# Kernel optimization log

Measured on AMD Instinct MI355X. Metric: run time of the kernel, lower is better.

## Reference

```python
import jax, jax.numpy as jnp
import numpy as np

B, K, H_IMG, W_IMG = 8, 1, 512, 512
N_ITR = 10      # fixed iteration count (torch max_itr loop, unrolled via scan)
TOL = 1e-3      # convergence tolerance used for per-element gating


def setup_inputs() -> dict:
    key = jax.random.key(0)
    k1, k2 = jax.random.split(key)
    img = jax.random.normal(k1, (B, K, H_IMG, W_IMG), dtype=jnp.float32)
    temp = jax.random.normal(k2, (B, K, H_IMG, W_IMG), dtype=jnp.float32)
    return {"img": img, "temp": temp}


def _grad_batch(F):
    # central difference with replicate padding (== conv with [-0.5,0,0.5])
    px = jnp.pad(F, ((0, 0), (0, 0), (0, 0), (1, 1)), mode='edge')
    dx = 0.5 * (px[..., 2:] - px[..., :-2])
    py = jnp.pad(F, ((0, 0), (0, 0), (1, 1), (0, 0)), mode='edge')
    dy = 0.5 * (py[..., 2:, :] - py[..., :-2, :])
    return dx, dy


def _bilinear_sample(img, xp, yp):
    # img [B,k,h,w]; xp,yp pixel coords [B,h,w]; zeros padding, align_corners=True
    _, k, h, w = img.shape
    x0 = jnp.floor(xp)
    y0 = jnp.floor(yp)
    wx1 = xp - x0
    wy1 = yp - y0

    def tap(xi, yi, wgt):
        valid = (xi >= 0) & (xi <= w - 1) & (yi >= 0) & (yi <= h - 1)
        xc = jnp.clip(xi, 0, w - 1).astype(jnp.int32)
        yc = jnp.clip(yi, 0, h - 1).astype(jnp.int32)
        v = jax.vmap(lambda im, yy, xx: im[:, yy, xx])(img, yc, xc)  # [B,k,h,w]
        return v * (wgt * valid.astype(img.dtype))[:, None]

    return (tap(x0, y0, (1 - wx1) * (1 - wy1)) + tap(x0 + 1, y0, wx1 * (1 - wy1))
            + tap(x0, y0 + 1, (1 - wx1) * wy1) + tap(x0 + 1, y0 + 1, wx1 * wy1))


def _deeplk(img, temp):
    Bb, k, h, w = temp.shape
    gx, gy = _grad_batch(temp)
    # centered pixel coordinates (meshgrid with x - x.max()/2)
    xs = jnp.arange(w, dtype=jnp.float32) - (w - 1) / 2.0
    ys = jnp.arange(h, dtype=jnp.float32) - (h - 1) / 2.0
    X, Y = jnp.meshgrid(xs, ys)  # each [h,w]
    Xf = jnp.tile(X.reshape(-1), k)  # [k*h*w]
    Yf = jnp.tile(Y.reshape(-1), k)
    gxf = gx.reshape(Bb, -1)
    gyf = gy.reshape(Bb, -1)
    # Jacobian dI/dp: [B, k*h*w, 8]
    dIdp = jnp.stack([
        Xf * gxf, Yf * gxf, gxf,
        Xf * gyf, Yf * gyf, gyf,
        -Xf * Xf * gxf - Xf * Yf * gyf,
        -Xf * Yf * gxf - Yf * Yf * gyf], axis=-1)
    Hm = jnp.einsum('bni,bnj->bij', dIdp, dIdp)        # [B,8,8]
    invH = jnp.linalg.inv(Hm)
    invH_dIdp = jnp.einsum('bij,bnj->bin', invH, dIdp)  # [B,8,N]

    xy1 = jnp.stack([X.reshape(-1), Y.reshape(-1),
                     jnp.ones(h * w, jnp.float32)], axis=0)  # [3, h*w]
    I3 = jnp.eye(3, dtype=jnp.float32)

    def param_to_H(p):
        return I3 + jnp.concatenate([p, jnp.zeros((Bb, 1), p.dtype)], 1).reshape(Bb, 3, 3)

    def step(carry, _):
        p, dp = carry  # p,dp: [B,8]
        Hh = param_to_H(p)
        xyw = jnp.einsum('bij,jn->bin', Hh, xy1)
        Xw = (xyw[:, 0] / xyw[:, 2]).reshape(Bb, h, w) + (w - 1) / 2.0
        Yw = (xyw[:, 1] / xyw[:, 2]).reshape(Bb, h, w) + (h - 1) / 2.0
        Fi_warp = _bilinear_sample(img, Xw, Yw)
        xn = Xw / ((w - 1) / 2.0) - 1.0
        yn = Yw / ((h - 1) / 2.0) - 1.0
        mask = ((xn > -1 + 2.0 / w) & (xn < 1 - 2.0 / w) &
                (yn > -1 + 2.0 / h) & (yn < 1 - 2.0 / h)).astype(img.dtype)
        r = (Fi_warp - temp * mask[:, None]).reshape(Bb, -1)  # [B,N]
        dp_new = jnp.einsum('bin,bn->bi', invH_dIdp, r)       # [B,8]
        dp_new = dp_new.at[:, 6:8].set(0.0)                   # no projective update
        gate = (jnp.linalg.norm(dp, axis=1, keepdims=True) > TOL).astype(p.dtype)
        dp_next = gate * dp_new
        return (p - dp_next, dp_next), None

    p0 = jnp.zeros((Bb, 8), jnp.float32)
    dp0 = jnp.ones((Bb, 8), jnp.float32)
    (p, _), _ = jax.lax.scan(step, (p0, dp0), None, length=N_ITR)
    return p.reshape(Bb, 8, 1), param_to_H(p)


def reference(img, temp):
    return _deeplk(img, temp)
```

## Files before the change

### kernel.cpp

```cpp
#include <hip/hip_runtime.h>
#include <math.h>

#define W     512
#define HH    512
#define NB    8
#define NBLK  512
#define TPB   512
#define NW    (TPB / 64)
#define BPB   64
#define ROWS  8
#define NPX   (ROWS * W)
#define PXT   (NPX / TPB)
#define NITR  10
#define POISON64 0xAAAAAAAAAAAAAAAAull
#define ALL64  0xFFFFFFFFFFFFFFFFull
#define MLO 0.998046875f
#define MHI 510.001953125f

__device__ __forceinline__ float wave_reduce8(float x) {
    x += __shfl_down(x, 32, 64);
    x += __shfl_down(x, 16, 64);
    x += __shfl_down(x, 8, 64);
    return x;
}
__device__ __forceinline__ double red8_d(double x) {
    x += __shfl_down(x, 32, 64);
    x += __shfl_down(x, 16, 64);
    x += __shfl_down(x, 8, 64);
    return x;
}
__device__ __forceinline__ double load_d(const double* p) {
    unsigned long long u = __hip_atomic_load((const unsigned long long*)p,
                       __ATOMIC_RELAXED, __HIP_MEMORY_SCOPE_AGENT);
    return __builtin_bit_cast(double, u);
}
__device__ __forceinline__ void store_d(double* p, double v) {
    __hip_atomic_store((unsigned long long*)p, __builtin_bit_cast(unsigned long long, v),
                       __ATOMIC_RELAXED, __HIP_MEMORY_SCOPE_AGENT);
}
__device__ __forceinline__ bool not_poison(double v) {
    return __builtin_bit_cast(unsigned long long, v) != POISON64;
}

__device__ __forceinline__ float hrec(int t, float X1, float X2, float X3, float X4,
    float a0, float a1, float a2, float b0, float b1, float b2, float b3,
    float c0, float c1, float c2, float c3, float c4)
{
    switch (t) {
    case 0:  return X2 * a0;             case 1:  return X1 * a1;
    case 2:  return X1 * a0;             case 3:  return X2 * b0;
    case 4:  return X1 * b1;             case 5:  return X1 * b0;
    case 6:  return -(X3 * a0 + X2 * b1);
    case 7:  return -(X2 * a1 + X1 * b2);
    case 8:  return a2;                  case 9:  return a1;
    case 10: return X1 * b1;             case 11: return b2;
    case 12: return b1;
    case 13: return -(X2 * a1 + X1 * b2);
    case 14: return -(X1 * a2 + b3);
    case 15: return a0;                  case 16: return X1 * b0;
    case 17: return b1;                  case 18: return b0;
    case 19: return -(X2 * a0 + X1 * b1);
    case 20: return -(X1 * a1 + b2);
    case 21: return X2 * c0;             case 22: return X1 * c1;
    case 23: return X1 * c0;
    case 24: return -(X3 * b0 + X2 * c1);
    case 25: return -(X2 * b1 + X1 * c2);
    case 26: return c2;                  case 27: return c1;
    case 28: return -(X2 * b1 + X1 * c2);
    case 29: return -(X1 * b2 + c3);
    case 30: return c0;
    case 31: return -(X2 * b0 + X1 * c1);
    case 32: return -(X1 * b1 + c2);
    case 33: return X4 * a0 + 2.f * X3 * b1 + X2 * c2;
    case 34: return X3 * a1 + 2.f * X2 * b2 + X1 * c3;
    default: return X2 * a2 + 2.f * X1 * b3 + c4;
    }
}

extern "C" __global__ __launch_bounds__(TPB, 4)
void deeplk_kernel(const float* __restrict__ img, const float* __restrict__ temp,
                   float* __restrict__ out, void* __restrict__ wsv)
{
    double* Hpart = (double*)wsv;
    double* vpart = Hpart + NB * 36 * BPB;

    const int tid   = threadIdx.x;
    const int lane  = tid & 63;
    const int wv    = tid >> 6;
    const int b     = blockIdx.x & 7;
    const int chunk = blockIdx.x >> 3;
    const int row0  = chunk * ROWS;
    const float* tb = temp + b * (HH * W);
    const float* ib = img  + b * (HH * W);

    float rgx[PXT], rgy[PXT], rtv[PXT];

    __shared__ float  s_h8[64 * 36];
    __shared__ float  s_h2[8 * 36];
    __shared__ double s_Hu[36];
    __shared__ double s_invH[64];
    __shared__ double s_p[8], s_dp[8], s_v[8];
    __shared__ double s_vred[8 * 8];

    const float X1 = (float)tid - 255.5f;

    float a0 = 0.f, a1 = 0.f, a2 = 0.f;
    float b0 = 0.f, b1 = 0.f, b2 = 0.f, b3 = 0.f;
    float c0 = 0.f, c1 = 0.f, c2 = 0.f, c3 = 0.f, c4 = 0.f;
    float A = 0.f, Bv = 0.f, Cv = 0.f, Dv = 0.f, Ev = 0.f;
    {
        const int cc = tid;
        const int cl = (cc > 0) ? cc - 1 : 0;
        const int cr = (cc < W - 1) ? cc + 1 : W - 1;
        const bool xm = (cc >= 1) && (cc <= 510);
        float Yv = (float)row0 - 255.5f;
#pragma unroll
        for (int u = 0; u < PXT; ++u) {
            const int rr = row0 + u;
            const int ru = (rr > 0) ? rr - 1 : 0;
            const int rd = (rr < HH - 1) ? rr + 1 : HH - 1;
            const float gx = 0.5f * (tb[rr * W + cr] - tb[rr * W + cl]);
            const float gy = 0.5f * (tb[rd * W + cc] - tb[ru * W + cc]);
            const float tc = tb[rr * W + cc];
            rgx[u] = gx; rgy[u] = gy; rtv[u] = tc;
            const float q1 = gx * gx, q2 = gx * gy, q3 = gy * gy;
            const float y2 = Yv * Yv, y3 = y2 * Yv, y4 = y2 * y2;
            a0 += q1; a1 += Yv * q1; a2 += y2 * q1;
            b0 += q2; b1 += Yv * q2; b2 += y2 * q2; b3 += y3 * q2;
            c0 += q3; c1 += Yv * q3; c2 += y2 * q3; c3 += y3 * q3; c4 += y4 * q3;
            const float m  = (xm && rr >= 1 && rr <= 510) ? 1.f : 0.f;
            const float rv = ib[rr * W + cc] - tc * m;
            const float t1 = gx * rv, t2 = gy * rv;
            A  += t1;        Bv += t2;
            Cv += Yv * t1;   Dv += Yv * t2;
            Ev += y2 * t2;
            Yv += 1.f;
        }
    }
    {
        const float X2 = X1 * X1, X3 = X2 * X1, X4 = X2 * X2;
#pragma unroll
        for (int t = 0; t < 36; ++t) {
            float x = wave_reduce8(hrec(t, X1, X2, X3, X4,
                                        a0, a1, a2, b0, b1, b2, b3,
                                        c0, c1, c2, c3, c4));
            if (lane < 8) s_h8[(wv * 8 + lane) * 36 + t] = x;
        }
        __syncthreads();
        if (tid < 288) {
            const int g = tid / 36, t = tid % 36;
            float s = 0.f;
#pragma unroll
            for (int w2 = 0; w2 < 8; ++w2) s += s_h8[(w2 * 8 + g) * 36 + t];
            s_h2[g * 36 + t] = s;
        }
        __syncthreads();
        if (tid < 36) {
            double s = 0.0;
#pragma unroll
            for (int g = 0; g < 8; ++g) s += (double)s_h2[g * 36 + tid];
            store_d(&Hpart[(b * 36 + tid) * BPB + chunk], s);
        }
        __syncthreads();
        float va[8];
        va[0] = X1 * A;  va[1] = Cv;  va[2] = A;
        va[3] = X1 * Bv; va[4] = Dv;  va[5] = Bv;
        va[6] = -(X1 * X1 * A + X1 * Dv);
        va[7] = -(X1 * Cv + Ev);
#pragma unroll
        for (int c = 0; c < 8; ++c) {
            float x = wave_reduce8(va[c]);
            if (lane < 8) s_h8[(wv * 8 + lane) * 8 + c] = x;
        }
        __syncthreads();
        if (tid < 64) {
            const int g = tid >> 3, c = tid & 7;
            float s = 0.f;
#pragma unroll
            for (int w2 = 0; w2 < 8; ++w2) s += s_h8[(w2 * 8 + g) * 8 + c];
            s_h2[g * 8 + c] = s;
        }
        __syncthreads();
        if (tid < 8) {
            double s = 0.0;
#pragma unroll
            for (int g = 0; g < 8; ++g) s += (double)s_h2[g * 8 + tid];
            store_d(&vpart[b * BPB * 8 + chunk * 8 + tid], s);
        }
    }
    for (int c = wv; c < 36; c += NW) {
        const double* hp = &Hpart[(b * 36 + c) * BPB + lane];
        double x;
        for (;;) {
            x = load_d(hp);
            if (__ballot(not_poison(x)) == ALL64) break;
            __builtin_amdgcn_s_sleep(1);
        }
        x += __shfl_down(x, 32, 64);
        x += __shfl_down(x, 16, 64);
        x += __shfl_down(x, 8, 64);
        x += __shfl_down(x, 4, 64);
        x += __shfl_down(x, 2, 64);
        x += __shfl_down(x, 1, 64);
        if (lane == 0) s_Hu[c] = x;
    }
    {
        const double* slot = &vpart[b * BPB * 8 + tid];
        double x;
        for (;;) {
            x = load_d(slot);
            if (__ballot(not_poison(x)) == ALL64) break;
            __builtin_amdgcn_s_sleep(1);
        }
        x += __shfl_down(x, 32, 64);
        x += __shfl_down(x, 16, 64);
        x += __shfl_down(x, 8, 64);
        if (lane < 8) s_vred[wv * 8 + lane] = x;
    }
    __syncthreads();
    if (tid < 8) {
        double s = 0.0;
#pragma unroll
        for (int w2 = 0; w2 < NW; ++w2) s += s_vred[w2 * 8 + tid];
        s_v[tid] = s;
    }
    __syncthreads();

    if (tid < 64) {
        const int r  = tid >> 3, cj = tid & 7;
        const int i2 = (r < cj) ? r : cj;
        const int j2 = (r < cj) ? cj : r;
        double a = s_Hu[i2 * 8 - (i2 * (i2 - 1)) / 2 + (j2 - i2)];
        double e = (r == cj) ? 1.0 : 0.0;
#pragma unroll
        for (int k = 0; k < 8; ++k) {
            int pr = k;
            double pv = fabs(__shfl(a, k * 8 + k, 64));
            for (int rr2 = k + 1; rr2 < 8; ++rr2) {
                double c = fabs(__shfl(a, rr2 * 8 + k, 64));
                if (c > pv) { pv = c; pr = rr2; }
            }
            double a_k = __shfl(a, k * 8 + cj, 64),  e_k = __shfl(e, k * 8 + cj, 64);
            double a_p = __shfl(a, pr * 8 + cj, 64), e_p = __shfl(e, pr * 8 + cj, 64);
            if (r == k)       { a = a_p; e = e_p; }
            else if (r == pr) { a = a_k; e = e_k; }
            double piv = __shfl(a, k * 8 + k, 64);
            double d = 1.0 / piv;
            if (r == k) { a *= d; e *= d; }
            double f  = __shfl(a, r * 8 + k, 64);
            double ak = __shfl(a, k * 8 + cj, 64);
            double ek = __shfl(e, k * 8 + cj, 64);
            if (r != k) { a -= f * ak; e -= f * ek; }
        }
        s_invH[tid] = e;
    }
    __syncthreads();
    if (tid < 8) {
        double dpn = 0.0;
#pragma unroll
        for (int l = 0; l < 8; ++l) dpn += s_invH[tid * 8 + l] * s_v[l];
        if (tid >= 6) dpn = 0.0;
        s_p[tid]  = -dpn;
        s_dp[tid] = dpn;
    }
    __syncthreads();

    for (int it = 1; it < NITR; ++it) {
        double n2 = 0.0;
#pragma unroll
        for (int l = 0; l < 8; ++l) { double d = s_dp[l]; n2 += d * d; }
        if (n2 > 1e-6) {
            const float a00 = 1.f + (float)s_p[0];
            const float a01 = (float)s_p[1];
            const float a02 = (float)s_p[2] + 255.5f;
            const float a10 = (float)s_p[3];
            const float a11 = 1.f + (float)s_p[4];
            const float a12 = (float)s_p[5] + 255.5f;
            float Yv = (float)row0 - 255.5f;
            float Xw = a00 * X1 + a01 * Yv + a02;
            float Yw = a10 * X1 + a11 * Yv + a12;
            float Ai = 0.f, Bi = 0.f, Ci = 0.f, Di = 0.f, Ei = 0.f;

#pragma unroll
            for (int u = 0; u < PXT; ++u) {
                const float xf = floorf(Xw), yf = floorf(Yw);
                const int ix = (int)xf, iy = (int)yf;
                const float wx = Xw - xf, wy = Yw - yf;
                const bool vx0 = (ix >= 0) & (ix < W);
                const bool vx1 = (ix >= -1) & (ix < W - 1);
                const bool vy0 = (iy >= 0) & (iy < HH);
                const bool vy1 = (iy >= -1) & (iy < HH - 1);
                const float* ro0 = ib + iy * W;
                const float* ro1 = ro0 + W;
                const float t00 = (vx0 && vy0) ? ro0[ix]     : 0.f;
                const float t10 = (vx1 && vy0) ? ro0[ix + 1] : 0.f;
                const float t01 = (vx0 && vy1) ? ro1[ix]     : 0.f;
                const float t11 = (vx1 && vy1) ? ro1[ix + 1] : 0.f;
                const float omx = 1.f - wx, omy = 1.f - wy;
                const float Fi = (t00 * omx + t10 * wx) * omy
                               + (t01 * omx + t11 * wx) * wy;
                const float m = (Xw > MLO && Xw < MHI && Yw > MLO && Yw < MHI) ? 1.f : 0.f;
                const float rv = Fi - rtv[u] * m;
                const float t1 = rgx[u] * rv, t2 = rgy[u] * rv;
                Ai += t1;        Bi += t2;
                Ci += Yv * t1;   Di += Yv * t2;
                Ei += (Yv * Yv) * t2;
                Xw += a01; Yw += a11; Yv += 1.f;
            }
            float va[8];
            {
                const float X2 = X1 * X1;
                va[0] = X1 * Ai; va[1] = Ci;  va[2] = Ai;
                va[3] = X1 * Bi; va[4] = Di;  va[5] = Bi;
                va[6] = -(X2 * Ai + X1 * Di);
                va[7] = -(X1 * Ci + Ei);
            }
#pragma unroll
            for (int c = 0; c < 8; ++c) {
                float x = wave_reduce8(va[c]);
                if (lane < 8) s_h8[(wv * 8 + lane) * 8 + c] = x;
            }
            __syncthreads();
            double* vp = vpart + ((it * NB) + b) * BPB * 8;
            if (wv == 0) {
                const int g2 = lane >> 3, c2 = lane & 7;
                double s = 0.0;
#pragma unroll
                for (int j = 0; j < 8; ++j) s += (double)s_h8[(j * 8 + g2) * 8 + c2];
                s = red8_d(s);
                if (lane < 8) store_d(&vp[chunk * 8 + lane], s);
            }
            {
                const double* slot = &vp[tid];
                double x;
                for (;;) {
                    x = load_d(slot);
                    if (__ballot(not_poison(x)) == ALL64) break;
                    __builtin_amdgcn_s_sleep(1);
                }
                x += __shfl_down(x, 32, 64);
                x += __shfl_down(x, 16, 64);
                x += __shfl_down(x, 8, 64);
                if (lane < 8) s_vred[wv * 8 + lane] = x;
            }
            __syncthreads();
            if (tid < 8) {
                double s = 0.0;
#pragma unroll
                for (int w2 = 0; w2 < NW; ++w2) s += s_vred[w2 * 8 + tid];
                s_v[tid] = s;
                double dpn = 0.0;
#pragma unroll
                for (int l = 0; l < 8; ++l) dpn += s_invH[tid * 8 + l] * s_v[l];
                if (tid >= 6) dpn = 0.0;
                s_p[tid] -= dpn;
                s_dp[tid] = dpn;
            }
            __syncthreads();
        }
    }

    if (chunk == 0) {
        if (tid < 8) out[b * 8 + tid] = (float)s_p[tid];
        if (tid == 0) {
            float* Ho = out + 64 + b * 9;
            Ho[0] = 1.f + (float)s_p[0]; Ho[1] = (float)s_p[1];       Ho[2] = (float)s_p[2];
            Ho[3] = (float)s_p[3];       Ho[4] = 1.f + (float)s_p[4]; Ho[5] = (float)s_p[5];
            Ho[6] = (float)s_p[6];       Ho[7] = (float)s_p[7];       Ho[8] = 1.f;
        }
    }
}

extern "C" void kernel_launch(void* const* d_in, const int* in_sizes, int n_in,
                              void* d_out, int out_size, void* d_ws, size_t ws_size,
                              hipStream_t stream) {
    const float* img  = (const float*)d_in[0];
    const float* temp = (const float*)d_in[1];
    float* out = (float*)d_out;
    void*  ws  = d_ws;
    void* args[] = { &img, &temp, &out, &ws };
    hipError_t e = hipLaunchCooperativeKernel((const void*)deeplk_kernel, dim3(NBLK),
                                              dim3(TPB), args, 0, stream);
    if (e != hipSuccess) {
        deeplk_kernel<<<dim3(NBLK), dim3(TPB), 0, stream>>>(img, temp, out, ws);
    }
}
```

Before: 152.0 us.

## Use 256 blocks of 1024 threads, each covering 16 rows

Halves the number of cooperating blocks by doubling the threads per block. Each block now covers 16 rows, split into two 8-row halves by thread index. The per-iteration cross-block spin-wait reduction then polls 32 partial slots per batch instead of 64, and the in-block reductions over 16 waves are adjusted to match. The aim is to cut global synchronisation and polling cost across the 10 iterations, at the price of fewer, larger blocks with higher register pressure. Launch bounds stay at (TPB, 4), so occupancy and register allocation may change.

```diff
diff --git a/kernel.cpp b/kernel.cpp
--- a/kernel.cpp
+++ b/kernel.cpp
@@ -4,11 +4,11 @@
 #define W     512
 #define HH    512
 #define NB    8
-#define NBLK  512
-#define TPB   512
+#define NBLK  256
+#define TPB   1024
 #define NW    (TPB / 64)
-#define BPB   64
-#define ROWS  8
+#define BPB   32
+#define ROWS  16
 #define NPX   (ROWS * W)
 #define PXT   (NPX / TPB)
 #define NITR  10
@@ -89,34 +89,35 @@
     const int wv    = tid >> 6;
     const int b     = blockIdx.x & 7;
     const int chunk = blockIdx.x >> 3;
-    const int row0  = chunk * ROWS;
+    const int cc    = tid & 511;
+    const int half  = tid >> 9;
+    const int rbase = chunk * ROWS + half * 8;
     const float* tb = temp + b * (HH * W);
     const float* ib = img  + b * (HH * W);
 
     float rgx[PXT], rgy[PXT], rtv[PXT];
 
-    __shared__ float  s_h8[64 * 36];
+    __shared__ float  s_h8[128 * 36];
     __shared__ float  s_h2[8 * 36];
     __shared__ double s_Hu[36];
     __shared__ double s_invH[64];
     __shared__ double s_p[8], s_dp[8], s_v[8];
     __shared__ double s_vred[8 * 8];
 
-    const float X1 = (float)tid - 255.5f;
+    const float X1 = (float)cc - 255.5f;
 
     float a0 = 0.f, a1 = 0.f, a2 = 0.f;
     float b0 = 0.f, b1 = 0.f, b2 = 0.f, b3 = 0.f;
     float c0 = 0.f, c1 = 0.f, c2 = 0.f, c3 = 0.f, c4 = 0.f;
     float A = 0.f, Bv = 0.f, Cv = 0.f, Dv = 0.f, Ev = 0.f;
     {
-        const int cc = tid;
         const int cl = (cc > 0) ? cc - 1 : 0;
         const int cr = (cc < W - 1) ? cc + 1 : W - 1;
         const bool xm = (cc >= 1) && (cc <= 510);
-        float Yv = (float)row0 - 255.5f;
+        float Yv = (float)rbase - 255.5f;
 #pragma unroll
         for (int u = 0; u < PXT; ++u) {
-            const int rr = row0 + u;
+            const int rr = rbase + u;
             const int ru = (rr > 0) ? rr - 1 : 0;
             const int rd = (rr < HH - 1) ? rr + 1 : HH - 1;
             const float gx = 0.5f * (tb[rr * W + cr] - tb[rr * W + cl]);
@@ -151,7 +152,7 @@
             const int g = tid / 36, t = tid % 36;
             float s = 0.f;
 #pragma unroll
-            for (int w2 = 0; w2 < 8; ++w2) s += s_h8[(w2 * 8 + g) * 36 + t];
+            for (int w2 = 0; w2 < 16; ++w2) s += s_h8[(w2 * 8 + g) * 36 + t];
             s_h2[g * 36 + t] = s;
         }
         __syncthreads();
@@ -177,7 +178,7 @@
             const int g = tid >> 3, c = tid & 7;
             float s = 0.f;
 #pragma unroll
-            for (int w2 = 0; w2 < 8; ++w2) s += s_h8[(w2 * 8 + g) * 8 + c];
+            for (int w2 = 0; w2 < 16; ++w2) s += s_h8[(w2 * 8 + g) * 8 + c];
             s_h2[g * 8 + c] = s;
         }
         __syncthreads();
@@ -189,14 +190,14 @@
         }
     }
     for (int c = wv; c < 36; c += NW) {
-        const double* hp = &Hpart[(b * 36 + c) * BPB + lane];
+        const double* hp = &Hpart[(b * 36 + c) * BPB + (lane & 31)];
         double x;
         for (;;) {
             x = load_d(hp);
             if (__ballot(not_poison(x)) == ALL64) break;
             __builtin_amdgcn_s_sleep(1);
         }
-        x += __shfl_down(x, 32, 64);
+        if (lane >= 32) x = 0.0;
         x += __shfl_down(x, 16, 64);
         x += __shfl_down(x, 8, 64);
         x += __shfl_down(x, 4, 64);
@@ -204,7 +205,7 @@
         x += __shfl_down(x, 1, 64);
         if (lane == 0) s_Hu[c] = x;
     }
-    {
+    if (tid < 256) {
         const double* slot = &vpart[b * BPB * 8 + tid];
         double x;
         for (;;) {
@@ -212,16 +213,14 @@
             if (__ballot(not_poison(x)) == ALL64) break;
             __builtin_amdgcn_s_sleep(1);
         }
-        x += __shfl_down(x, 32, 64);
-        x += __shfl_down(x, 16, 64);
-        x += __shfl_down(x, 8, 64);
+        x = red8_d(x);
         if (lane < 8) s_vred[wv * 8 + lane] = x;
     }
     __syncthreads();
     if (tid < 8) {
         double s = 0.0;
 #pragma unroll
-        for (int w2 = 0; w2 < NW; ++w2) s += s_vred[w2 * 8 + tid];
+        for (int w2 = 0; w2 < 4; ++w2) s += s_vred[w2 * 8 + tid];
         s_v[tid] = s;
     }
     __syncthreads();
@@ -276,7 +275,7 @@
             const float a10 = (float)s_p[3];
             const float a11 = 1.f + (float)s_p[4];
             const float a12 = (float)s_p[5] + 255.5f;
-            float Yv = (float)row0 - 255.5f;
+            float Yv = (float)rbase - 255.5f;
             float Xw = a00 * X1 + a01 * Yv + a02;
             float Yw = a10 * X1 + a11 * Yv + a12;
             float Ai = 0.f, Bi = 0.f, Ci = 0.f, Di = 0.f, Ei = 0.f;
@@ -326,11 +325,11 @@
                 const int g2 = lane >> 3, c2 = lane & 7;
                 double s = 0.0;
 #pragma unroll
-                for (int j = 0; j < 8; ++j) s += (double)s_h8[(j * 8 + g2) * 8 + c2];
+                for (int j = 0; j < 16; ++j) s += (double)s_h8[(j * 8 + g2) * 8 + c2];
                 s = red8_d(s);
                 if (lane < 8) store_d(&vp[chunk * 8 + lane], s);
             }
-            {
+            if (tid < 256) {
                 const double* slot = &vp[tid];
                 double x;
                 for (;;) {
@@ -338,16 +337,14 @@
                     if (__ballot(not_poison(x)) == ALL64) break;
                     __builtin_amdgcn_s_sleep(1);
                 }
-                x += __shfl_down(x, 32, 64);
-                x += __shfl_down(x, 16, 64);
-                x += __shfl_down(x, 8, 64);
+                x = red8_d(x);
                 if (lane < 8) s_vred[wv * 8 + lane] = x;
             }
             __syncthreads();
             if (tid < 8) {
                 double s = 0.0;
 #pragma unroll
-                for (int w2 = 0; w2 < NW; ++w2) s += s_vred[w2 * 8 + tid];
+                for (int w2 = 0; w2 < 4; ++w2) s += s_vred[w2 * 8 + tid];
                 s_v[tid] = s;
                 double dpn = 0.0;
 #pragma unroll
```

New measurement: 143.8 us. -5.4%, faster.
